# Kernel optimization log

Measured on AMD Instinct MI355X. Metric: run time of the kernel, lower is better.

## Reference

```python
import jax, jax.numpy as jnp
import numpy as np

H, KV, D, HID = 16, 8, 128, 2048  # n_heads, n_kv_heads, head_dim, hidden_size
EPS = 1e-6
SCALE = D ** -0.5


def rotate_half(x):
    x1, x2 = x[..., : x.shape[-1] // 2], x[..., x.shape[-1] // 2 :]
    return jnp.concatenate((-x2, x1), axis=-1)


def rms_norm(x, w, eps=EPS):
    xf = x.astype(jnp.float32)
    xf = xf * jax.lax.rsqrt(jnp.mean(jnp.square(xf), axis=-1, keepdims=True) + eps)
    return (w * xf).astype(x.dtype)


def setup_inputs() -> dict:
    key = jax.random.key(0)
    ks = jax.random.split(key, 8)
    B, S = 2, 2048
    x = jax.random.normal(ks[0], (B, S, HID), dtype=jnp.float32)
    # RoPE tables from rope_theta frequencies
    theta = 5e6
    inv_freq = 1.0 / (theta ** (np.arange(0, D, 2, dtype=np.float32) / D))  # (D/2,)
    pos = np.arange(S, dtype=np.float32)
    freqs = np.outer(pos, inv_freq)  # (S, D/2)
    emb = np.concatenate([freqs, freqs], axis=-1)  # (S, D)
    sin = jnp.broadcast_to(jnp.asarray(np.sin(emb)), (B, S, D)).astype(jnp.float32)
    cos = jnp.broadcast_to(jnp.asarray(np.cos(emb)), (B, S, D)).astype(jnp.float32)
    # causal additive mask (B, 1, S, S)
    causal = jnp.where(jnp.tril(jnp.ones((S, S), dtype=bool)), 0.0, -1e9).astype(jnp.float32)
    attention_mask = jnp.broadcast_to(causal[None, None], (B, 1, S, S))
    std = 0.02
    Wq = jax.random.normal(ks[1], (HID, H * D), dtype=jnp.float32) * std
    Wk = jax.random.normal(ks[2], (HID, KV * D), dtype=jnp.float32) * std
    Wv = jax.random.normal(ks[3], (HID, KV * D), dtype=jnp.float32) * std
    Wo = jax.random.normal(ks[4], (H * D, HID), dtype=jnp.float32) * std
    q_norm_w = jnp.ones((D,), dtype=jnp.float32)
    k_norm_w = jnp.ones((D,), dtype=jnp.float32)
    return dict(x=x, sin=sin, cos=cos, attention_mask=attention_mask,
                Wq=Wq, Wk=Wk, Wv=Wv, Wo=Wo, q_norm_w=q_norm_w, k_norm_w=k_norm_w)


def reference(x, sin, cos, attention_mask, Wq, Wk, Wv, Wo, q_norm_w, k_norm_w):
    B, S, _ = x.shape
    groups = H // KV
    q = (x @ Wq).reshape(B, S, H, D)
    k = (x @ Wk).reshape(B, S, KV, D)
    v = (x @ Wv).reshape(B, S, KV, D)
    q = rms_norm(q, q_norm_w)
    k = rms_norm(k, k_norm_w)
    c, s = cos[:, :, None, :], sin[:, :, None, :]
    q = q * c + rotate_half(q) * s
    k = k * c + rotate_half(k) * s
    if groups > 1:
        k = jnp.repeat(k, groups, axis=2)  # (B,S,H,D)
        v = jnp.repeat(v, groups, axis=2)
    attn = jnp.einsum('bihd,bjhd->bhij', q, k) * SCALE  # (B,H,S,S)
    attn = jax.nn.softmax(attn + attention_mask, axis=-1)
    out = jnp.einsum('bhij,bjhd->bihd', attn, v).reshape(B, S, H * D)
    return out @ Wo
```

## Files before the change

kernel.cpp:

```cpp
#include <hip/hip_runtime.h>
#include <hip/hip_bf16.h>
#include <math.h>

#define H_    16
#define KV_   8
#define D_    128
#define HID_  2048
#define NQKV_ 4096
#define SCALE_ 0.08838834764831845f

typedef __attribute__((ext_vector_type(8))) short bf16x8;
typedef __attribute__((ext_vector_type(4))) float f32x4;
typedef __attribute__((ext_vector_type(4))) short short4v;

__device__ inline unsigned short f2bf(float f) {
  unsigned u = __builtin_bit_cast(unsigned, f);
  u += 0x7FFF + ((u >> 16) & 1);
  return (unsigned short)(u >> 16);
}

#define GLDS16(g, l)                                                     \
  __builtin_amdgcn_global_load_lds(                                      \
      (const __attribute__((address_space(1))) void*)(g),                \
      (__attribute__((address_space(3))) void*)(l), 16, 0, 0)

__global__ __launch_bounds__(256) void f32_to_bf16(
    const float* __restrict__ in, unsigned short* __restrict__ out, int n8) {
  int i = blockIdx.x * 256 + threadIdx.x;
  if (i >= n8) return;
  const float4* p = (const float4*)in + (size_t)i * 2;
  float4 a = p[0], b = p[1];
  unsigned short o[8] = {f2bf(a.x), f2bf(a.y), f2bf(a.z), f2bf(a.w),
                         f2bf(b.x), f2bf(b.y), f2bf(b.z), f2bf(b.w)};
  *(bf16x8*)(out + (size_t)i * 8) = *(bf16x8*)o;
}

__global__ __launch_bounds__(256) void transpose_bf16(
    const float* __restrict__ in, unsigned short* __restrict__ out, int K, int N) {
  __shared__ float t[32][33];
  const int k0 = blockIdx.y * 32, n0 = blockIdx.x * 32;
  const int r = threadIdx.x >> 3, c4 = (threadIdx.x & 7) * 4;
  float4 v = *(const float4*)(in + (size_t)(k0 + r) * N + n0 + c4);
  t[r][c4 + 0] = v.x; t[r][c4 + 1] = v.y; t[r][c4 + 2] = v.z; t[r][c4 + 3] = v.w;
  __syncthreads();
  unsigned short o[4];
#pragma unroll
  for (int j = 0; j < 4; ++j) o[j] = f2bf(t[c4 + j][r]);
  *(short4v*)(out + (size_t)(n0 + r) * K + k0 + c4) = *(short4v*)o;
}

__global__ __launch_bounds__(256) void transpose_qkv3(
    const float* __restrict__ Wq, const float* __restrict__ Wk,
    const float* __restrict__ Wv, unsigned short* __restrict__ out) {
  __shared__ float t[32][33];
  const int n0 = blockIdx.x * 32;
  const int k0 = blockIdx.y * 32;
  const float* src; int N, nloc;
  if (n0 < H_ * D_)                  { src = Wq; N = H_ * D_;  nloc = n0; }
  else if (n0 < H_ * D_ + KV_ * D_)  { src = Wk; N = KV_ * D_; nloc = n0 - H_ * D_; }
  else                               { src = Wv; N = KV_ * D_; nloc = n0 - H_ * D_ - KV_ * D_; }
  const int r = threadIdx.x >> 3, c4 = (threadIdx.x & 7) * 4;
  float4 v = *(const float4*)(src + (size_t)(k0 + r) * N + nloc + c4);
  t[r][c4 + 0] = v.x; t[r][c4 + 1] = v.y; t[r][c4 + 2] = v.z; t[r][c4 + 3] = v.w;
  __syncthreads();
  unsigned short o[4];
#pragma unroll
  for (int j = 0; j < 4; ++j) o[j] = f2bf(t[c4 + j][r]);
  *(short4v*)(out + (size_t)(n0 + r) * HID_ + k0 + c4) = *(short4v*)o;
}

#define QBM 256
#define QBN 256
#define QBK 64

template <int EPI>
__global__ __launch_bounds__(512, 2) void gemm256(
    const unsigned short* __restrict__ A,
    const unsigned short* __restrict__ Bt,
    float* __restrict__ C0, float* __restrict__ C1,
    unsigned short* __restrict__ C2, int M, int N, int K, int S) {
  __shared__ unsigned short As[2][QBM * QBK];
  __shared__ unsigned short Bs[2][QBN * QBK];
  const int tid = threadIdx.x;
  const int w = tid >> 6, lane = tid & 63;
  const int wm = w >> 2, wn = w & 3;
  const int fr = lane & 15, fq = lane >> 4;
  const int row0 = blockIdx.y * QBM, col0 = blockIdx.x * QBN;

  const unsigned short* Ab = A + (size_t)row0 * K;
  const unsigned short* Bb = Bt + (size_t)col0 * K;
  const int srow = w * 8 + (lane >> 3);
  const int sc   = lane & 7;
  const int nt   = K / QBK;

  f32x4 acc[8][4] = {};

#define STAGE256(t_, buf_)                                                      \
  {                                                                             \
    const int k0_ = (t_) * QBK;                                                 \
    _Pragma("unroll")                                                           \
    for (int p = 0; p < 4; ++p) {                                               \
      const int r_ = p * 64 + srow;                                             \
      const int gc_ = sc ^ (r_ & 7);                                            \
      GLDS16(Ab + (size_t)r_ * K + k0_ + gc_ * 8,                               \
             &As[buf_][(p * 64 + w * 8) * QBK]);                                \
      GLDS16(Bb + (size_t)r_ * K + k0_ + gc_ * 8,                               \
             &Bs[buf_][(p * 64 + w * 8) * QBK]);                                \
    }                                                                           \
  }

  STAGE256(0, 0);
  STAGE256(1, 1);
  asm volatile("s_waitcnt vmcnt(8)" ::: "memory");
  __builtin_amdgcn_s_barrier();
  __builtin_amdgcn_sched_barrier(0);

  for (int t = 0; t < nt; ++t) {
    const int buf = t & 1;
    __builtin_amdgcn_s_setprio(1);
#pragma unroll
    for (int s = 0; s < 2; ++s) {
      bf16x8 af[8], bf[4];
#pragma unroll
      for (int i = 0; i < 8; ++i) {
        const int r = wm * 128 + i * 16 + fr;
        af[i] = *(const bf16x8*)(&As[buf][r * QBK + (((s << 2) | fq) ^ (r & 7)) * 8]);
      }
#pragma unroll
      for (int j = 0; j < 4; ++j) {
        const int r = wn * 64 + j * 16 + fr;
        bf[j] = *(const bf16x8*)(&Bs[buf][r * QBK + (((s << 2) | fq) ^ (r & 7)) * 8]);
      }
#pragma unroll
      for (int i = 0; i < 8; ++i)
#pragma unroll
        for (int j = 0; j < 4; ++j)
          acc[i][j] = __builtin_amdgcn_mfma_f32_16x16x32_bf16(af[i], bf[j], acc[i][j], 0, 0, 0);
    }
    __builtin_amdgcn_s_setprio(0);
    __builtin_amdgcn_sched_barrier(0);
    __builtin_amdgcn_s_barrier();
    if (t + 2 < nt) {
      STAGE256(t + 2, buf);
      asm volatile("s_waitcnt vmcnt(8)" ::: "memory");
    } else {
      asm volatile("s_waitcnt vmcnt(0)" ::: "memory");
    }
    __builtin_amdgcn_s_barrier();
    __builtin_amdgcn_sched_barrier(0);
  }

  if constexpr (EPI == 0) {
#pragma unroll
    for (int i = 0; i < 8; ++i)
#pragma unroll
      for (int j = 0; j < 4; ++j) {
        const int col = col0 + wn * 64 + j * 16 + fr;
#pragma unroll
        for (int r = 0; r < 4; ++r) {
          const int row = row0 + wm * 128 + i * 16 + fq * 4 + r;
          C0[(size_t)row * N + col] = acc[i][j][r];
        }
      }
  } else {
    if (col0 < H_ * D_) {
#pragma unroll
      for (int i = 0; i < 8; ++i)
#pragma unroll
        for (int j = 0; j < 4; ++j) {
          const int col = col0 + wn * 64 + j * 16 + fr;
#pragma unroll
          for (int r = 0; r < 4; ++r) {
            const int row = row0 + wm * 128 + i * 16 + fq * 4 + r;
            C0[(size_t)row * (H_ * D_) + col] = acc[i][j][r];
          }
        }
    } else if (col0 < H_ * D_ + KV_ * D_) {
#pragma unroll
      for (int i = 0; i < 8; ++i)
#pragma unroll
        for (int j = 0; j < 4; ++j) {
          const int col = col0 - H_ * D_ + wn * 64 + j * 16 + fr;
#pragma unroll
          for (int r = 0; r < 4; ++r) {
            const int row = row0 + wm * 128 + i * 16 + fq * 4 + r;
            C1[(size_t)row * (KV_ * D_) + col] = acc[i][j][r];
          }
        }
    } else {
#pragma unroll
      for (int i = 0; i < 8; ++i)
#pragma unroll
        for (int j = 0; j < 4; ++j) {
          const int cc = col0 - (H_ * D_ + KV_ * D_) + wn * 64 + j * 16 + fr;
          const int kvh = cc >> 7, d = cc & 127;
          const int row = row0 + wm * 128 + i * 16 + fq * 4;
          const int b = row / S, s = row - b * S;
          unsigned short o[4] = {f2bf(acc[i][j][0]), f2bf(acc[i][j][1]),
                                 f2bf(acc[i][j][2]), f2bf(acc[i][j][3])};
          *(short4v*)(C2 + ((size_t)(b * KV_ + kvh) * D_ + d) * S + s) = *(short4v*)o;
        }
    }
  }
#undef STAGE256
}

__global__ __launch_bounds__(256) void rmsnorm_rope_o16(
    const float* __restrict__ p, unsigned short* __restrict__ o16,
    const float* __restrict__ w, const float* __restrict__ cs,
    const float* __restrict__ sn, int nheads, float oscale) {
  const int row  = blockIdx.x * 4 + (threadIdx.x >> 6);
  const int lane = threadIdx.x & 63;
  const float* base = p + (size_t)row * D_;
  float x1 = base[lane];
  float x2 = base[lane + 64];
  float ss = x1 * x1 + x2 * x2;
#pragma unroll
  for (int m = 32; m; m >>= 1) ss += __shfl_xor(ss, m);
  float r = rsqrtf(ss * (1.0f / 128.0f) + 1e-6f);
  const size_t sidx = (size_t)(row / nheads) * D_;
  float n1 = x1 * r * w[lane];
  float n2 = x2 * r * w[lane + 64];
  unsigned short* ob = o16 + (size_t)row * D_;
  ob[lane]      = f2bf((n1 * cs[sidx + lane]      - n2 * sn[sidx + lane])      * oscale);
  ob[lane + 64] = f2bf((n2 * cs[sidx + lane + 64] + n1 * sn[sidx + lane + 64]) * oscale);
}

__global__ __launch_bounds__(256) void flash_bf16(
    const unsigned short* __restrict__ Qb, const unsigned short* __restrict__ Kb,
    const unsigned short* __restrict__ Vt, unsigned short* __restrict__ O,
    int S, int nqt) {
  __shared__ unsigned short Kt[128 * 128];
  __shared__ unsigned short Vs[128 * 128];
  __shared__ unsigned short Pl[4][16 * 128];
  const int h = blockIdx.y, b = blockIdx.z;
  const int kvh = h >> 1;
  const int tid = threadIdx.x, w = tid >> 6, lane = tid & 63;
  const int fr = lane & 15, fq = lane >> 4;
  const int rl = lane >> 4;
  const int sch = lane & 15;
  const unsigned short* vhead = Vt + (size_t)(b * KV_ + kvh) * D_ * S;

#pragma unroll 1
  for (int half = 0; half < 2; ++half) {
    const int qt = half ? (nqt - 1 - (int)blockIdx.x) : (int)blockIdx.x;
    const int q0 = qt * 64;
    const int nkt = (q0 + 64 + 127) >> 7;

    bf16x8 qf[4];
    {
      const unsigned short* qp =
          Qb + ((size_t)(b * S + q0 + w * 16 + fr) * H_ + h) * D_;
#pragma unroll
      for (int s = 0; s < 4; ++s) qf[s] = *(const bf16x8*)(qp + s * 32 + fq * 8);
    }

    f32x4 acco[8] = {};
    float mrow[4] = {-1e30f, -1e30f, -1e30f, -1e30f};
    float lrow[4] = {0.f, 0.f, 0.f, 0.f};

#pragma unroll 1
    for (int kt = 0; kt < nkt; ++kt) {
      __syncthreads();
#pragma unroll
      for (int p = 0; p < 8; ++p) {
        const int r = p * 16 + w * 4 + rl;
        const int gch = (sch & 8) | ((sch ^ r) & 7);
        GLDS16(Kb + ((size_t)(b * S + kt * 128 + r) * KV_ + kvh) * D_ + gch * 8,
               Kt + (p * 16 + w * 4) * 128);
        GLDS16(vhead + (size_t)r * S + kt * 128 + gch * 8,
               Vs + (p * 16 + w * 4) * 128);
      }
      __syncthreads();

      f32x4 sa[8];
      __builtin_amdgcn_s_setprio(1);
#pragma unroll
      for (int t = 0; t < 8; ++t) {
        f32x4 a = {};
        const int kv = 16 * t + fr;
#pragma unroll
        for (int s = 0; s < 4; ++s) {
          const int ch = 4 * s + fq;
          const int chs = (ch & 8) | ((ch ^ kv) & 7);
          bf16x8 kf = *(const bf16x8*)(Kt + kv * 128 + chs * 8);
          a = __builtin_amdgcn_mfma_f32_16x16x32_bf16(qf[s], kf, a, 0, 0, 0);
        }
        sa[t] = a;
      }
      __builtin_amdgcn_s_setprio(0);

      if (kt == nkt - 1) {
#pragma unroll
        for (int t = 0; t < 8; ++t) {
          const int kvg = kt * 128 + 16 * t + fr;
#pragma unroll
          for (int r = 0; r < 4; ++r)
            if (kvg > q0 + w * 16 + fq * 4 + r) sa[t][r] = -1e30f;
        }
      }

      float al[4];
#pragma unroll
      for (int r = 0; r < 4; ++r) {
        float mx = sa[0][r];
#pragma unroll
        for (int t = 1; t < 8; ++t) mx = fmaxf(mx, sa[t][r]);
        mx = fmaxf(mx, __shfl_xor(mx, 1));
        mx = fmaxf(mx, __shfl_xor(mx, 2));
        mx = fmaxf(mx, __shfl_xor(mx, 4));
        mx = fmaxf(mx, __shfl_xor(mx, 8));
        const float mn = fmaxf(mrow[r], mx);
        al[r] = __expf(mrow[r] - mn);
        mrow[r] = mn;
        float sum = 0.f;
#pragma unroll
        for (int t = 0; t < 8; ++t) {
          const float pv = __expf(sa[t][r] - mn);
          sa[t][r] = pv;
          sum += pv;
        }
        sum += __shfl_xor(sum, 1);
        sum += __shfl_xor(sum, 2);
        sum += __shfl_xor(sum, 4);
        sum += __shfl_xor(sum, 8);
        lrow[r] = lrow[r] * al[r] + sum;
#pragma unroll
        for (int c = 0; c < 8; ++c) acco[c][r] *= al[r];
      }

      unsigned short* pw = &Pl[w][0];
#pragma unroll
      for (int t = 0; t < 8; ++t) {
        const int kv = 16 * t + fr;
        const int ch = kv >> 3;
#pragma unroll
        for (int r = 0; r < 4; ++r) {
          const int q = fq * 4 + r;
          pw[q * 128 + ((ch & 8) | ((ch ^ q) & 7)) * 8 + (kv & 7)] = f2bf(sa[t][r]);
        }
      }

      bf16x8 pf[4];
#pragma unroll
      for (int s = 0; s < 4; ++s) {
        const int ch = 4 * s + fq;
        pf[s] = *(const bf16x8*)(pw + fr * 128 + ((ch & 8) | ((ch ^ fr) & 7)) * 8);
      }
      __builtin_amdgcn_s_setprio(1);
#pragma unroll
      for (int c = 0; c < 8; ++c) {
        const int d = 16 * c + fr;
#pragma unroll
        for (int s = 0; s < 4; ++s) {
          const int ch = 4 * s + fq;
          bf16x8 vf = *(const bf16x8*)(Vs + d * 128 + ((ch & 8) | ((ch ^ d) & 7)) * 8);
          acco[c] = __builtin_amdgcn_mfma_f32_16x16x32_bf16(pf[s], vf, acco[c], 0, 0, 0);
        }
      }
      __builtin_amdgcn_s_setprio(0);
    }

    float inv[4];
#pragma unroll
    for (int r = 0; r < 4; ++r) inv[r] = 1.0f / lrow[r];
#pragma unroll
    for (int c = 0; c < 8; ++c) {
#pragma unroll
      for (int r = 0; r < 4; ++r) {
        const int q = q0 + w * 16 + fq * 4 + r;
        O[(size_t)(b * S + q) * (H_ * D_) + h * D_ + 16 * c + fr] =
            f2bf(acco[c][r] * inv[r]);
      }
    }
  }
}

extern "C" void kernel_launch(void* const* d_in, const int* in_sizes, int n_in,
                              void* d_out, int out_size, void* d_ws, size_t ws_size,
                              hipStream_t stream) {
  const float* x  = (const float*)d_in[0];
  const float* sn = (const float*)d_in[1];
  const float* cs = (const float*)d_in[2];
  const float* Wq = (const float*)d_in[4];
  const float* Wk = (const float*)d_in[5];
  const float* Wv = (const float*)d_in[6];
  const float* Wo = (const float*)d_in[7];
  const float* qw = (const float*)d_in[8];
  const float* kw = (const float*)d_in[9];
  float* out = (float*)d_out;

  const int BS = in_sizes[0] / HID_;
  const int S  = in_sizes[3] / BS;
  const int B  = BS / S;

  float* kbuf = (float*)d_ws;
  unsigned short* vt   = (unsigned short*)(kbuf + (size_t)BS * KV_ * D_);
  unsigned short* xb   = vt + (size_t)BS * KV_ * D_;
  unsigned short* wT   = xb + (size_t)BS * HID_;
  unsigned short* qb   = wT + (size_t)NQKV_ * HID_;
  unsigned short* kb16 = qb + (size_t)BS * H_ * D_;
  unsigned short* ab16 = xb;

  dim3 blk(256);
  const int n8x = BS * HID_ / 8;

  f32_to_bf16<<<dim3(n8x / 256), blk, 0, stream>>>(x, xb, n8x);

  transpose_qkv3<<<dim3(NQKV_ / 32, HID_ / 32), blk, 0, stream>>>(Wq, Wk, Wv, wT);

  gemm256<1><<<dim3(NQKV_ / QBN, BS / QBM), dim3(512), 0, stream>>>(
      xb, wT, out, kbuf, vt, BS, NQKV_, HID_, S);

  rmsnorm_rope_o16<<<dim3(BS * H_ / 4),  blk, 0, stream>>>(out,  qb,   qw, cs, sn, H_,  SCALE_);
  rmsnorm_rope_o16<<<dim3(BS * KV_ / 4), blk, 0, stream>>>(kbuf, kb16, kw, cs, sn, KV_, 1.0f);

  flash_bf16<<<dim3(S / 128, H_, B), blk, 0, stream>>>(qb, kb16, vt, ab16, S, S / 64);

  transpose_bf16<<<dim3(HID_ / 32, (H_ * D_) / 32), blk, 0, stream>>>(Wo, wT, H_ * D_, HID_);
  gemm256<0><<<dim3(HID_ / QBN, BS / QBM), dim3(512), 0, stream>>>(
      ab16, wT, out, nullptr, nullptr, BS, HID_, HID_, S);
}
```

Measured before the change: 398.9 us.

## Double-buffer flash attention, skip lazy rescale, fuse Q/K norm, remap GEMM blocks

The flash attention kernel now uses 512 threads with 128-query blocks and 64-key tiles. K/V tiles are double-buffered through async global-to-LDS loads so the next tile loads while the current one computes. It also skips the output rescale when the running max grows by no more than a threshold. Separately, the Q and K rmsnorm/rope launches are merged into one kernel, and GEMM block IDs are permuted to spread neighbouring tiles across XCDs. These aim to hide load latency and cut launch and softmax overhead, at the cost of more LDS, more barriers and bounded-overflow assumptions in the exp.

Measured after the change: 407.3 us. 2.1% more time.

```diff
diff --git a/kernel.cpp b/kernel.cpp
--- a/kernel.cpp
+++ b/kernel.cpp
@@ -85,7 +85,11 @@
   const int w = tid >> 6, lane = tid & 63;
   const int wm = w >> 2, wn = w & 3;
   const int fr = lane & 15, fq = lane >> 4;
-  const int row0 = blockIdx.y * QBM, col0 = blockIdx.x * QBN;
+  const int nwg = gridDim.x * gridDim.y;
+  const int bid0 = blockIdx.y * gridDim.x + blockIdx.x;
+  const int bid = (bid0 & 7) * (nwg >> 3) + (bid0 >> 3);
+  const int bx = bid % gridDim.x, by = bid / gridDim.x;
+  const int row0 = by * QBM, col0 = bx * QBN;
 
   const unsigned short* Ab = A + (size_t)row0 * K;
   const unsigned short* Bb = Bt + (size_t)col0 * K;
@@ -205,12 +209,16 @@
 #undef STAGE256
 }
 
-__global__ __launch_bounds__(256) void rmsnorm_rope_o16(
-    const float* __restrict__ p, unsigned short* __restrict__ o16,
-    const float* __restrict__ w, const float* __restrict__ cs,
-    const float* __restrict__ sn, int nheads, float oscale) {
-  const int row  = blockIdx.x * 4 + (threadIdx.x >> 6);
+__global__ __launch_bounds__(256) void rmsnorm_rope2(
+    const float* __restrict__ qsrc, const float* __restrict__ ksrc,
+    unsigned short* __restrict__ qdst, unsigned short* __restrict__ kdst,
+    const float* __restrict__ qw, const float* __restrict__ kw,
+    const float* __restrict__ cs, const float* __restrict__ sn, int qrows) {
+  int row = blockIdx.x * 4 + (threadIdx.x >> 6);
   const int lane = threadIdx.x & 63;
+  const float* p; unsigned short* o16; const float* w; int nheads; float oscale;
+  if (row < qrows) { p = qsrc; o16 = qdst; w = qw; nheads = H_;  oscale = SCALE_; }
+  else { row -= qrows; p = ksrc; o16 = kdst; w = kw; nheads = KV_; oscale = 1.0f; }
   const float* base = p + (size_t)row * D_;
   float x1 = base[lane];
   float x2 = base[lane + 64];
@@ -226,26 +234,45 @@
   ob[lane + 64] = f2bf((n2 * cs[sidx + lane + 64] + n1 * sn[sidx + lane + 64]) * oscale);
 }
 
-__global__ __launch_bounds__(256) void flash_bf16(
+__global__ __launch_bounds__(512) void flash_bf16(
     const unsigned short* __restrict__ Qb, const unsigned short* __restrict__ Kb,
-    const unsigned short* __restrict__ Vt, unsigned short* __restrict__ O,
-    int S, int nqt) {
-  __shared__ unsigned short Kt[128 * 128];
-  __shared__ unsigned short Vs[128 * 128];
-  __shared__ unsigned short Pl[4][16 * 128];
+    const unsigned short* __restrict__ Vt, unsigned short* __restrict__ O, int S) {
+  __shared__ unsigned short Kt[2][64 * 128];
+  __shared__ unsigned short Vs[2][128 * 64];
+  __shared__ unsigned short Pl[8][16 * 64];
   const int h = blockIdx.y, b = blockIdx.z;
   const int kvh = h >> 1;
   const int tid = threadIdx.x, w = tid >> 6, lane = tid & 63;
   const int fr = lane & 15, fq = lane >> 4;
-  const int rl = lane >> 4;
-  const int sch = lane & 15;
+  const int nqb = S >> 7;
   const unsigned short* vhead = Vt + (size_t)(b * KV_ + kvh) * D_ * S;
+
+#define FSTAGE(t_, buf_)                                                        \
+  {                                                                             \
+    const int kv0_ = (t_) * 64;                                                 \
+    _Pragma("unroll")                                                           \
+    for (int p = 0; p < 2; ++p) {                                               \
+      const int rk_ = p * 32 + w * 4 + (lane >> 4);                             \
+      const int ck_ = lane & 15;                                                \
+      const int gk_ = (ck_ & 8) | ((ck_ ^ rk_) & 7);                            \
+      GLDS16(Kb + ((size_t)(b * S + kv0_ + rk_) * KV_ + kvh) * D_ + gk_ * 8,    \
+             &Kt[buf_][(p * 32 + w * 4) * 128]);                                \
+    }                                                                           \
+    _Pragma("unroll")                                                           \
+    for (int p = 0; p < 2; ++p) {                                               \
+      const int rv_ = p * 64 + w * 8 + (lane >> 3);                             \
+      const int cv_ = lane & 7;                                                 \
+      const int gv_ = cv_ ^ (rv_ & 7);                                          \
+      GLDS16(vhead + (size_t)rv_ * S + kv0_ + gv_ * 8,                          \
+             &Vs[buf_][(p * 64 + w * 8) * 64]);                                 \
+    }                                                                           \
+  }
 
 #pragma unroll 1
   for (int half = 0; half < 2; ++half) {
-    const int qt = half ? (nqt - 1 - (int)blockIdx.x) : (int)blockIdx.x;
-    const int q0 = qt * 64;
-    const int nkt = (q0 + 64 + 127) >> 7;
+    const int qb = half ? (nqb - 1 - (int)blockIdx.x) : (int)blockIdx.x;
+    const int q0 = qb * 128;
+    const int nkt = 2 * qb + 2;
 
     bf16x8 qf[4];
     {
@@ -259,106 +286,132 @@
     float mrow[4] = {-1e30f, -1e30f, -1e30f, -1e30f};
     float lrow[4] = {0.f, 0.f, 0.f, 0.f};
 
+    FSTAGE(0, 0);
+    FSTAGE(1, 1);
+    asm volatile("s_waitcnt vmcnt(4)" ::: "memory");
+    __builtin_amdgcn_s_barrier();
+    __builtin_amdgcn_sched_barrier(0);
+
 #pragma unroll 1
     for (int kt = 0; kt < nkt; ++kt) {
-      __syncthreads();
-#pragma unroll
-      for (int p = 0; p < 8; ++p) {
-        const int r = p * 16 + w * 4 + rl;
-        const int gch = (sch & 8) | ((sch ^ r) & 7);
-        GLDS16(Kb + ((size_t)(b * S + kt * 128 + r) * KV_ + kvh) * D_ + gch * 8,
-               Kt + (p * 16 + w * 4) * 128);
-        GLDS16(vhead + (size_t)r * S + kt * 128 + gch * 8,
-               Vs + (p * 16 + w * 4) * 128);
-      }
-      __syncthreads();
-
-      f32x4 sa[8];
+      const int buf = kt & 1;
+
+      f32x4 sa[4];
       __builtin_amdgcn_s_setprio(1);
 #pragma unroll
-      for (int t = 0; t < 8; ++t) {
+      for (int t = 0; t < 4; ++t) {
         f32x4 a = {};
         const int kv = 16 * t + fr;
 #pragma unroll
         for (int s = 0; s < 4; ++s) {
           const int ch = 4 * s + fq;
           const int chs = (ch & 8) | ((ch ^ kv) & 7);
-          bf16x8 kf = *(const bf16x8*)(Kt + kv * 128 + chs * 8);
+          bf16x8 kf = *(const bf16x8*)(&Kt[buf][kv * 128 + chs * 8]);
           a = __builtin_amdgcn_mfma_f32_16x16x32_bf16(qf[s], kf, a, 0, 0, 0);
         }
         sa[t] = a;
       }
       __builtin_amdgcn_s_setprio(0);
 
-      if (kt == nkt - 1) {
-#pragma unroll
-        for (int t = 0; t < 8; ++t) {
-          const int kvg = kt * 128 + 16 * t + fr;
+      if (kt >= 2 * qb) {
+#pragma unroll
+        for (int t = 0; t < 4; ++t) {
+          const int kvg = kt * 64 + 16 * t + fr;
 #pragma unroll
           for (int r = 0; r < 4; ++r)
             if (kvg > q0 + w * 16 + fq * 4 + r) sa[t][r] = -1e30f;
         }
       }
 
-      float al[4];
+      float mx[4];
 #pragma unroll
       for (int r = 0; r < 4; ++r) {
-        float mx = sa[0][r];
-#pragma unroll
-        for (int t = 1; t < 8; ++t) mx = fmaxf(mx, sa[t][r]);
-        mx = fmaxf(mx, __shfl_xor(mx, 1));
-        mx = fmaxf(mx, __shfl_xor(mx, 2));
-        mx = fmaxf(mx, __shfl_xor(mx, 4));
-        mx = fmaxf(mx, __shfl_xor(mx, 8));
-        const float mn = fmaxf(mrow[r], mx);
-        al[r] = __expf(mrow[r] - mn);
-        mrow[r] = mn;
-        float sum = 0.f;
-#pragma unroll
-        for (int t = 0; t < 8; ++t) {
-          const float pv = __expf(sa[t][r] - mn);
-          sa[t][r] = pv;
-          sum += pv;
-        }
-        sum += __shfl_xor(sum, 1);
-        sum += __shfl_xor(sum, 2);
-        sum += __shfl_xor(sum, 4);
-        sum += __shfl_xor(sum, 8);
-        lrow[r] = lrow[r] * al[r] + sum;
-#pragma unroll
-        for (int c = 0; c < 8; ++c) acco[c][r] *= al[r];
+        float m = fmaxf(fmaxf(sa[0][r], sa[1][r]), fmaxf(sa[2][r], sa[3][r]));
+        m = fmaxf(m, __shfl_xor(m, 1));
+        m = fmaxf(m, __shfl_xor(m, 2));
+        m = fmaxf(m, __shfl_xor(m, 4));
+        m = fmaxf(m, __shfl_xor(m, 8));
+        mx[r] = m;
+      }
+      const bool nogrow = (mx[0] <= mrow[0] + 8.f) & (mx[1] <= mrow[1] + 8.f) &
+                          (mx[2] <= mrow[2] + 8.f) & (mx[3] <= mrow[3] + 8.f);
+      if (__all(nogrow)) {
+#pragma unroll
+        for (int r = 0; r < 4; ++r) {
+          float sum = 0.f;
+#pragma unroll
+          for (int t = 0; t < 4; ++t) {
+            const float pv = __expf(sa[t][r] - mrow[r]);
+            sa[t][r] = pv;
+            sum += pv;
+          }
+          sum += __shfl_xor(sum, 1);
+          sum += __shfl_xor(sum, 2);
+          sum += __shfl_xor(sum, 4);
+          sum += __shfl_xor(sum, 8);
+          lrow[r] += sum;
+        }
+      } else {
+#pragma unroll
+        for (int r = 0; r < 4; ++r) {
+          const float mn = fmaxf(mrow[r], mx[r]);
+          const float al = __expf(mrow[r] - mn);
+          mrow[r] = mn;
+          float sum = 0.f;
+#pragma unroll
+          for (int t = 0; t < 4; ++t) {
+            const float pv = __expf(sa[t][r] - mn);
+            sa[t][r] = pv;
+            sum += pv;
+          }
+          sum += __shfl_xor(sum, 1);
+          sum += __shfl_xor(sum, 2);
+          sum += __shfl_xor(sum, 4);
+          sum += __shfl_xor(sum, 8);
+          lrow[r] = lrow[r] * al + sum;
+#pragma unroll
+          for (int c = 0; c < 8; ++c) acco[c][r] *= al;
+        }
       }
 
       unsigned short* pw = &Pl[w][0];
 #pragma unroll
-      for (int t = 0; t < 8; ++t) {
+      for (int t = 0; t < 4; ++t) {
         const int kv = 16 * t + fr;
         const int ch = kv >> 3;
 #pragma unroll
         for (int r = 0; r < 4; ++r) {
           const int q = fq * 4 + r;
-          pw[q * 128 + ((ch & 8) | ((ch ^ q) & 7)) * 8 + (kv & 7)] = f2bf(sa[t][r]);
-        }
-      }
-
-      bf16x8 pf[4];
-#pragma unroll
-      for (int s = 0; s < 4; ++s) {
-        const int ch = 4 * s + fq;
-        pf[s] = *(const bf16x8*)(pw + fr * 128 + ((ch & 8) | ((ch ^ fr) & 7)) * 8);
-      }
+          pw[q * 64 + ((ch ^ q) & 7) * 8 + (kv & 7)] = f2bf(sa[t][r]);
+        }
+      }
+
+      bf16x8 pf[2];
+#pragma unroll
+      for (int s = 0; s < 2; ++s)
+        pf[s] = *(const bf16x8*)(pw + fr * 64 + (((4 * s + fq) ^ fr) & 7) * 8);
       __builtin_amdgcn_s_setprio(1);
 #pragma unroll
       for (int c = 0; c < 8; ++c) {
         const int d = 16 * c + fr;
 #pragma unroll
-        for (int s = 0; s < 4; ++s) {
-          const int ch = 4 * s + fq;
-          bf16x8 vf = *(const bf16x8*)(Vs + d * 128 + ((ch & 8) | ((ch ^ d) & 7)) * 8);
+        for (int s = 0; s < 2; ++s) {
+          bf16x8 vf = *(const bf16x8*)(&Vs[buf][d * 64 + (((4 * s + fq) ^ d) & 7) * 8]);
           acco[c] = __builtin_amdgcn_mfma_f32_16x16x32_bf16(pf[s], vf, acco[c], 0, 0, 0);
         }
       }
       __builtin_amdgcn_s_setprio(0);
+
+      __builtin_amdgcn_sched_barrier(0);
+      __builtin_amdgcn_s_barrier();
+      if (kt + 2 < nkt) {
+        FSTAGE(kt + 2, buf);
+        asm volatile("s_waitcnt vmcnt(4)" ::: "memory");
+      } else {
+        asm volatile("s_waitcnt vmcnt(0)" ::: "memory");
+      }
+      __builtin_amdgcn_s_barrier();
+      __builtin_amdgcn_sched_barrier(0);
     }
 
     float inv[4];
@@ -374,6 +427,7 @@
       }
     }
   }
+#undef FSTAGE
 }
 
 extern "C" void kernel_launch(void* const* d_in, const int* in_sizes, int n_in,
@@ -412,10 +466,10 @@
   gemm256<1><<<dim3(NQKV_ / QBN, BS / QBM), dim3(512), 0, stream>>>(
       xb, wT, out, kbuf, vt, BS, NQKV_, HID_, S);
 
-  rmsnorm_rope_o16<<<dim3(BS * H_ / 4),  blk, 0, stream>>>(out,  qb,   qw, cs, sn, H_,  SCALE_);
-  rmsnorm_rope_o16<<<dim3(BS * KV_ / 4), blk, 0, stream>>>(kbuf, kb16, kw, cs, sn, KV_, 1.0f);
-
-  flash_bf16<<<dim3(S / 128, H_, B), blk, 0, stream>>>(qb, kb16, vt, ab16, S, S / 64);
+  rmsnorm_rope2<<<dim3((BS * H_ + BS * KV_) / 4), blk, 0, stream>>>(
+      out, kbuf, qb, kb16, qw, kw, cs, sn, BS * H_);
+
+  flash_bf16<<<dim3(S / 256, H_, B), dim3(512), 0, stream>>>(qb, kb16, vt, ab16, S);
 
   transpose_bf16<<<dim3(HID_ / 32, (H_ * D_) / 32), blk, 0, stream>>>(Wo, wT, H_ * D_, HID_);
   gemm256<0><<<dim3(HID_ / QBN, BS / QBM), dim3(512), 0, stream>>>(
```

## Fuse prep and norm kernels, remap GEMM/flash block order, skip softmax rescale

Applied to the files above, without the earlier changes.

Merges the x conversion and all three weight transposes, Wo included, into one prep_all launch, and merges the Q and K RMSNorm+RoPE launches into one. GEMM workgroup IDs are remapped across 8 groups, which looks aimed at XCD locality. Flash blocks are flattened so the two query heads sharing a KV head sit next to each other. Softmax skips the running-max update and the accumulator rescale when the new tile max grows by no more than 8, which trades fewer exps and multiplies for exponents that can reach up to e^8. It also uses extra workspace for a separate Wo buffer.

New measurement: 424.5 us. 1.06x slower.

```diff
diff --git a/kernel.cpp b/kernel.cpp
--- a/kernel.cpp
+++ b/kernel.cpp
@@ -24,49 +24,50 @@
       (const __attribute__((address_space(1))) void*)(g),                \
       (__attribute__((address_space(3))) void*)(l), 16, 0, 0)
 
-__global__ __launch_bounds__(256) void f32_to_bf16(
-    const float* __restrict__ in, unsigned short* __restrict__ out, int n8) {
-  int i = blockIdx.x * 256 + threadIdx.x;
-  if (i >= n8) return;
-  const float4* p = (const float4*)in + (size_t)i * 2;
-  float4 a = p[0], b = p[1];
-  unsigned short o[8] = {f2bf(a.x), f2bf(a.y), f2bf(a.z), f2bf(a.w),
-                         f2bf(b.x), f2bf(b.y), f2bf(b.z), f2bf(b.w)};
-  *(bf16x8*)(out + (size_t)i * 8) = *(bf16x8*)o;
-}
-
-__global__ __launch_bounds__(256) void transpose_bf16(
-    const float* __restrict__ in, unsigned short* __restrict__ out, int K, int N) {
+__global__ __launch_bounds__(256) void prep_all(
+    const float* __restrict__ x, unsigned short* __restrict__ xb,
+    const float* __restrict__ Wq, const float* __restrict__ Wk,
+    const float* __restrict__ Wv, unsigned short* __restrict__ wT,
+    const float* __restrict__ Wo, unsigned short* __restrict__ wTo) {
+  const int bid = blockIdx.x;
+  if (bid < 4096) {
+    const int i = bid * 256 + threadIdx.x;
+    const float4* p = (const float4*)x + (size_t)i * 2;
+    float4 a = p[0], b = p[1];
+    unsigned short o[8] = {f2bf(a.x), f2bf(a.y), f2bf(a.z), f2bf(a.w),
+                           f2bf(b.x), f2bf(b.y), f2bf(b.z), f2bf(b.w)};
+    *(bf16x8*)(xb + (size_t)i * 8) = *(bf16x8*)o;
+    return;
+  }
   __shared__ float t[32][33];
-  const int k0 = blockIdx.y * 32, n0 = blockIdx.x * 32;
   const int r = threadIdx.x >> 3, c4 = (threadIdx.x & 7) * 4;
-  float4 v = *(const float4*)(in + (size_t)(k0 + r) * N + n0 + c4);
-  t[r][c4 + 0] = v.x; t[r][c4 + 1] = v.y; t[r][c4 + 2] = v.z; t[r][c4 + 3] = v.w;
-  __syncthreads();
-  unsigned short o[4];
-#pragma unroll
-  for (int j = 0; j < 4; ++j) o[j] = f2bf(t[c4 + j][r]);
-  *(short4v*)(out + (size_t)(n0 + r) * K + k0 + c4) = *(short4v*)o;
-}
-
-__global__ __launch_bounds__(256) void transpose_qkv3(
-    const float* __restrict__ Wq, const float* __restrict__ Wk,
-    const float* __restrict__ Wv, unsigned short* __restrict__ out) {
-  __shared__ float t[32][33];
-  const int n0 = blockIdx.x * 32;
-  const int k0 = blockIdx.y * 32;
-  const float* src; int N, nloc;
-  if (n0 < H_ * D_)                  { src = Wq; N = H_ * D_;  nloc = n0; }
-  else if (n0 < H_ * D_ + KV_ * D_)  { src = Wk; N = KV_ * D_; nloc = n0 - H_ * D_; }
-  else                               { src = Wv; N = KV_ * D_; nloc = n0 - H_ * D_ - KV_ * D_; }
-  const int r = threadIdx.x >> 3, c4 = (threadIdx.x & 7) * 4;
-  float4 v = *(const float4*)(src + (size_t)(k0 + r) * N + nloc + c4);
-  t[r][c4 + 0] = v.x; t[r][c4 + 1] = v.y; t[r][c4 + 2] = v.z; t[r][c4 + 3] = v.w;
-  __syncthreads();
-  unsigned short o[4];
-#pragma unroll
-  for (int j = 0; j < 4; ++j) o[j] = f2bf(t[c4 + j][r]);
-  *(short4v*)(out + (size_t)(n0 + r) * HID_ + k0 + c4) = *(short4v*)o;
+  if (bid < 12288) {
+    const int b2 = bid - 4096;
+    const int n0 = (b2 & 127) * 32;
+    const int k0 = (b2 >> 7) * 32;
+    const float* src; int N, nloc;
+    if (n0 < H_ * D_)                  { src = Wq; N = H_ * D_;  nloc = n0; }
+    else if (n0 < H_ * D_ + KV_ * D_)  { src = Wk; N = KV_ * D_; nloc = n0 - H_ * D_; }
+    else                               { src = Wv; N = KV_ * D_; nloc = n0 - H_ * D_ - KV_ * D_; }
+    float4 v = *(const float4*)(src + (size_t)(k0 + r) * N + nloc + c4);
+    t[r][c4 + 0] = v.x; t[r][c4 + 1] = v.y; t[r][c4 + 2] = v.z; t[r][c4 + 3] = v.w;
+    __syncthreads();
+    unsigned short o[4];
+#pragma unroll
+    for (int j = 0; j < 4; ++j) o[j] = f2bf(t[c4 + j][r]);
+    *(short4v*)(wT + (size_t)(n0 + r) * HID_ + k0 + c4) = *(short4v*)o;
+  } else {
+    const int b3 = bid - 12288;
+    const int n0 = (b3 & 63) * 32;
+    const int k0 = (b3 >> 6) * 32;
+    float4 v = *(const float4*)(Wo + (size_t)(k0 + r) * HID_ + n0 + c4);
+    t[r][c4 + 0] = v.x; t[r][c4 + 1] = v.y; t[r][c4 + 2] = v.z; t[r][c4 + 3] = v.w;
+    __syncthreads();
+    unsigned short o[4];
+#pragma unroll
+    for (int j = 0; j < 4; ++j) o[j] = f2bf(t[c4 + j][r]);
+    *(short4v*)(wTo + (size_t)(n0 + r) * (H_ * D_) + k0 + c4) = *(short4v*)o;
+  }
 }
 
 #define QBM 256
@@ -85,7 +86,11 @@
   const int w = tid >> 6, lane = tid & 63;
   const int wm = w >> 2, wn = w & 3;
   const int fr = lane & 15, fq = lane >> 4;
-  const int row0 = blockIdx.y * QBM, col0 = blockIdx.x * QBN;
+  const int nwg = gridDim.x * gridDim.y;
+  const int bid0 = blockIdx.y * gridDim.x + blockIdx.x;
+  const int bid = (bid0 & 7) * (nwg >> 3) + (bid0 >> 3);
+  const int bx = bid % gridDim.x, by = bid / gridDim.x;
+  const int row0 = by * QBM, col0 = bx * QBN;
 
   const unsigned short* Ab = A + (size_t)row0 * K;
   const unsigned short* Bb = Bt + (size_t)col0 * K;
@@ -205,12 +210,16 @@
 #undef STAGE256
 }
 
-__global__ __launch_bounds__(256) void rmsnorm_rope_o16(
-    const float* __restrict__ p, unsigned short* __restrict__ o16,
-    const float* __restrict__ w, const float* __restrict__ cs,
-    const float* __restrict__ sn, int nheads, float oscale) {
-  const int row  = blockIdx.x * 4 + (threadIdx.x >> 6);
+__global__ __launch_bounds__(256) void rmsnorm_rope2(
+    const float* __restrict__ qsrc, const float* __restrict__ ksrc,
+    unsigned short* __restrict__ qdst, unsigned short* __restrict__ kdst,
+    const float* __restrict__ qw, const float* __restrict__ kw,
+    const float* __restrict__ cs, const float* __restrict__ sn, int qrows) {
+  int row = blockIdx.x * 4 + (threadIdx.x >> 6);
   const int lane = threadIdx.x & 63;
+  const float* p; unsigned short* o16; const float* w; int nheads; float oscale;
+  if (row < qrows) { p = qsrc; o16 = qdst; w = qw; nheads = H_;  oscale = SCALE_; }
+  else { row -= qrows; p = ksrc; o16 = kdst; w = kw; nheads = KV_; oscale = 1.0f; }
   const float* base = p + (size_t)row * D_;
   float x1 = base[lane];
   float x2 = base[lane + 64];
@@ -233,8 +242,13 @@
   __shared__ unsigned short Kt[128 * 128];
   __shared__ unsigned short Vs[128 * 128];
   __shared__ unsigned short Pl[4][16 * 128];
-  const int h = blockIdx.y, b = blockIdx.z;
-  const int kvh = h >> 1;
+  const int fid = blockIdx.x;
+  const int kvh = fid & 7;
+  const int rest = fid >> 3;
+  const int b = rest >> 5;
+  const int j = rest & 31;
+  const int qpair = j & 15;
+  const int h = kvh * 2 + (j >> 4);
   const int tid = threadIdx.x, w = tid >> 6, lane = tid & 63;
   const int fr = lane & 15, fq = lane >> 4;
   const int rl = lane >> 4;
@@ -243,7 +257,7 @@
 
 #pragma unroll 1
   for (int half = 0; half < 2; ++half) {
-    const int qt = half ? (nqt - 1 - (int)blockIdx.x) : (int)blockIdx.x;
+    const int qt = half ? (nqt - 1 - qpair) : qpair;
     const int q0 = qt * 64;
     const int nkt = (q0 + 64 + 127) >> 7;
 
@@ -300,33 +314,57 @@
         }
       }
 
-      float al[4];
+      float mx[4];
 #pragma unroll
       for (int r = 0; r < 4; ++r) {
-        float mx = sa[0][r];
-#pragma unroll
-        for (int t = 1; t < 8; ++t) mx = fmaxf(mx, sa[t][r]);
-        mx = fmaxf(mx, __shfl_xor(mx, 1));
-        mx = fmaxf(mx, __shfl_xor(mx, 2));
-        mx = fmaxf(mx, __shfl_xor(mx, 4));
-        mx = fmaxf(mx, __shfl_xor(mx, 8));
-        const float mn = fmaxf(mrow[r], mx);
-        al[r] = __expf(mrow[r] - mn);
-        mrow[r] = mn;
-        float sum = 0.f;
-#pragma unroll
-        for (int t = 0; t < 8; ++t) {
-          const float pv = __expf(sa[t][r] - mn);
-          sa[t][r] = pv;
-          sum += pv;
-        }
-        sum += __shfl_xor(sum, 1);
-        sum += __shfl_xor(sum, 2);
-        sum += __shfl_xor(sum, 4);
-        sum += __shfl_xor(sum, 8);
-        lrow[r] = lrow[r] * al[r] + sum;
-#pragma unroll
-        for (int c = 0; c < 8; ++c) acco[c][r] *= al[r];
+        float m = sa[0][r];
+#pragma unroll
+        for (int t = 1; t < 8; ++t) m = fmaxf(m, sa[t][r]);
+        m = fmaxf(m, __shfl_xor(m, 1));
+        m = fmaxf(m, __shfl_xor(m, 2));
+        m = fmaxf(m, __shfl_xor(m, 4));
+        m = fmaxf(m, __shfl_xor(m, 8));
+        mx[r] = m;
+      }
+      const bool nogrow = (mx[0] <= mrow[0] + 8.f) & (mx[1] <= mrow[1] + 8.f) &
+                          (mx[2] <= mrow[2] + 8.f) & (mx[3] <= mrow[3] + 8.f);
+      if (__all(nogrow)) {
+#pragma unroll
+        for (int r = 0; r < 4; ++r) {
+          float sum = 0.f;
+#pragma unroll
+          for (int t = 0; t < 8; ++t) {
+            const float pv = __expf(sa[t][r] - mrow[r]);
+            sa[t][r] = pv;
+            sum += pv;
+          }
+          sum += __shfl_xor(sum, 1);
+          sum += __shfl_xor(sum, 2);
+          sum += __shfl_xor(sum, 4);
+          sum += __shfl_xor(sum, 8);
+          lrow[r] += sum;
+        }
+      } else {
+#pragma unroll
+        for (int r = 0; r < 4; ++r) {
+          const float mn = fmaxf(mrow[r], mx[r]);
+          const float al = __expf(mrow[r] - mn);
+          mrow[r] = mn;
+          float sum = 0.f;
+#pragma unroll
+          for (int t = 0; t < 8; ++t) {
+            const float pv = __expf(sa[t][r] - mn);
+            sa[t][r] = pv;
+            sum += pv;
+          }
+          sum += __shfl_xor(sum, 1);
+          sum += __shfl_xor(sum, 2);
+          sum += __shfl_xor(sum, 4);
+          sum += __shfl_xor(sum, 8);
+          lrow[r] = lrow[r] * al + sum;
+#pragma unroll
+          for (int c = 0; c < 8; ++c) acco[c][r] *= al;
+        }
       }
 
       unsigned short* pw = &Pl[w][0];
@@ -398,26 +436,23 @@
   unsigned short* vt   = (unsigned short*)(kbuf + (size_t)BS * KV_ * D_);
   unsigned short* xb   = vt + (size_t)BS * KV_ * D_;
   unsigned short* wT   = xb + (size_t)BS * HID_;
-  unsigned short* qb   = wT + (size_t)NQKV_ * HID_;
+  unsigned short* wTo  = wT + (size_t)NQKV_ * HID_;
+  unsigned short* qb   = wTo + (size_t)HID_ * (H_ * D_);
   unsigned short* kb16 = qb + (size_t)BS * H_ * D_;
   unsigned short* ab16 = xb;
 
   dim3 blk(256);
-  const int n8x = BS * HID_ / 8;
-
-  f32_to_bf16<<<dim3(n8x / 256), blk, 0, stream>>>(x, xb, n8x);
-
-  transpose_qkv3<<<dim3(NQKV_ / 32, HID_ / 32), blk, 0, stream>>>(Wq, Wk, Wv, wT);
+
+  prep_all<<<dim3(16384), blk, 0, stream>>>(x, xb, Wq, Wk, Wv, wT, Wo, wTo);
 
   gemm256<1><<<dim3(NQKV_ / QBN, BS / QBM), dim3(512), 0, stream>>>(
       xb, wT, out, kbuf, vt, BS, NQKV_, HID_, S);
 
-  rmsnorm_rope_o16<<<dim3(BS * H_ / 4),  blk, 0, stream>>>(out,  qb,   qw, cs, sn, H_,  SCALE_);
-  rmsnorm_rope_o16<<<dim3(BS * KV_ / 4), blk, 0, stream>>>(kbuf, kb16, kw, cs, sn, KV_, 1.0f);
-
-  flash_bf16<<<dim3(S / 128, H_, B), blk, 0, stream>>>(qb, kb16, vt, ab16, S, S / 64);
-
-  transpose_bf16<<<dim3(HID_ / 32, (H_ * D_) / 32), blk, 0, stream>>>(Wo, wT, H_ * D_, HID_);
+  rmsnorm_rope2<<<dim3((BS * H_ + BS * KV_) / 4), blk, 0, stream>>>(
+      out, kbuf, qb, kb16, qw, kw, cs, sn, BS * H_);
+
+  flash_bf16<<<dim3((S / 128) * H_ * B), blk, 0, stream>>>(qb, kb16, vt, ab16, S, S / 64);
+
   gemm256<0><<<dim3(HID_ / QBN, BS / QBM), dim3(512), 0, stream>>>(
-      ab16, wT, out, nullptr, nullptr, BS, HID_, HID_, S);
-}
+      ab16, wTo, out, nullptr, nullptr, BS, HID_, HID_, S);
+}
```
